# Kernel tuning notes

Hardware: AMD Instinct MI355X
Metric: run time of the kernel (lower is better)

The kernel has to match this reference:

```python
import jax, jax.numpy as jnp
import numpy as np


def _run_stacked_lstm(x, init_hc, params):
    """x: [B,T,E]; init_hc: tuple of (h,c) per layer; params: tuple of (W,U,b) per layer.
    Keras LSTMCell gate order: i, f, g(candidate), o; sigmoid recurrent act, tanh act."""
    def step(carry, xt):
        inp = xt
        new = []
        for (h, c), (W, U, b) in zip(carry, params):
            z = inp @ W + h @ U + b                      # [B, 4*units]
            i, f, g, o = jnp.split(z, 4, axis=-1)
            c2 = jax.nn.sigmoid(f) * c + jax.nn.sigmoid(i) * jnp.tanh(g)
            h2 = jax.nn.sigmoid(o) * jnp.tanh(c2)
            new.append((h2, c2))
            inp = h2                                     # feed to next layer
        return tuple(new), inp
    carry, ys = jax.lax.scan(step, init_hc, jnp.swapaxes(x, 0, 1))
    return jnp.swapaxes(ys, 0, 1), carry                 # [B,T,units], final states


def setup_inputs() -> dict:
    key = jax.random.key(0)
    ks = jax.random.split(key, 20)
    B, T, V, E, H, L = 16, 64, 32000, 512, 512, 2
    s = 0.02
    inp = {
        'ids_1': jax.random.randint(ks[0], (B, T), 0, V),
        'ids_2': jax.random.randint(ks[1], (B, T), 0, V),
        'init_state': jax.random.normal(ks[2], (L, B, H), jnp.float32),
        'emb': jax.random.normal(ks[3], (V, E), jnp.float32) * s,
        'W1_0': jax.random.normal(ks[4], (E, 4 * H), jnp.float32) * s,
        'U1_0': jax.random.normal(ks[5], (H, 4 * H), jnp.float32) * s,
        'b1_0': jnp.zeros((4 * H,), jnp.float32),
        'W1_1': jax.random.normal(ks[6], (H, 4 * H), jnp.float32) * s,
        'U1_1': jax.random.normal(ks[7], (H, 4 * H), jnp.float32) * s,
        'b1_1': jnp.zeros((4 * H,), jnp.float32),
        'W2_0': jax.random.normal(ks[8], (E, 8 * H), jnp.float32) * s,
        'U2_0': jax.random.normal(ks[9], (2 * H, 8 * H), jnp.float32) * s,
        'b2_0': jnp.zeros((8 * H,), jnp.float32),
        'W2_1': jax.random.normal(ks[10], (2 * H, 8 * H), jnp.float32) * s,
        'U2_1': jax.random.normal(ks[11], (2 * H, 8 * H), jnp.float32) * s,
        'b2_1': jnp.zeros((8 * H,), jnp.float32),
        'Wp1': jax.random.normal(ks[12], (H, V), jnp.float32) * s,
        'bp1': jnp.zeros((V,), jnp.float32),
        'Wp2': jax.random.normal(ks[13], (2 * H, V), jnp.float32) * s,
        'bp2': jnp.zeros((V,), jnp.float32),
    }
    return inp


def reference(ids_1, ids_2, init_state, emb,
              W1_0, U1_0, b1_0, W1_1, U1_1, b1_1,
              W2_0, U2_0, b2_0, W2_1, U2_1, b2_1,
              Wp1, bp1, Wp2, bp2):
    L = init_state.shape[0]
    e1 = emb[ids_1]                                       # [B,T,E]
    e2 = emb[ids_2]
    # RNN1: initial (h,c) both set to init_state per layer
    init1 = tuple((init_state[l], init_state[l]) for l in range(L))
    p1 = ((W1_0, U1_0, b1_0), (W1_1, U1_1, b1_1))
    out1, st1 = _run_stacked_lstm(e1, init1, p1)
    logits1 = out1 @ Wp1 + bp1                            # [B,T,V]
    # RNN2: initial h = concat(init, h1_final), c = concat(init, c1_final)
    init2 = tuple((jnp.concatenate([init_state[l], st1[l][0]], axis=1),
                   jnp.concatenate([init_state[l], st1[l][1]], axis=1))
                  for l in range(L))
    p2 = ((W2_0, U2_0, b2_0), (W2_1, U2_1, b2_1))
    out2, _ = _run_stacked_lstm(e2, init2, p2)
    logits2 = out2 @ Wp2 + bp2                            # [B,T,V]
    return (logits1, logits2)
```

## Files before the change

### kernel.cpp

```cpp
#include <hip/hip_runtime.h>
#include <hip/hip_bf16.h>

#define B_ 16
#define T_ 64
#define E_ 512
#define H_ 512
#define V_ 32000

typedef __attribute__((ext_vector_type(4))) float f32x4;
typedef __attribute__((ext_vector_type(8))) short s16x8;

__device__ __forceinline__ float sigm(float x){ return 1.0f/(1.0f + __expf(-x)); }

__device__ __forceinline__ unsigned short f2bf(float x){
  unsigned int u = __float_as_uint(x);
  return (unsigned short)((u + 0x7FFFu + ((u>>16)&1u)) >> 16);
}

__device__ __forceinline__ unsigned load_coh(const unsigned* p){
  unsigned v;
  asm volatile("global_load_dword %0, %1, off sc0 sc1\n\ts_waitcnt vmcnt(0)"
               : "=v"(v) : "v"(p) : "memory");
  return v;
}
__device__ __forceinline__ void store_coh16(unsigned short* p, unsigned v){
  asm volatile("global_store_short %0, %1, off sc0 sc1" :: "v"(p), "v"(v) : "memory");
}
__device__ __forceinline__ void store_cohf(float* p, float v){
  asm volatile("global_store_dword %0, %1, off sc0 sc1" :: "v"(p), "v"(v) : "memory");
}
__device__ __forceinline__ void store_cohu(unsigned* p, unsigned v){
  asm volatile("global_store_dword %0, %1, off sc0 sc1" :: "v"(p), "v"(v) : "memory");
}

__device__ __forceinline__ void gbar3(unsigned* barb, unsigned bi1, int nblk,
                                      bool det, int myblk){
  asm volatile("s_waitcnt vmcnt(0)" ::: "memory");
  __syncthreads();
  const int tid = threadIdx.x;
  if(tid == 0) store_cohu(barb + (size_t)myblk*16, bi1);
  if(det){
    if(tid < nblk){
      const unsigned* fp = barb + (size_t)tid*16;
      while(load_coh(fp) < bi1) __builtin_amdgcn_s_sleep(1);
    }
    __syncthreads();
    if(tid < 8) store_cohu(barb + 4096 + (size_t)tid*16, bi1);
  } else {
    if(tid == 0){
      const unsigned* gp = barb + 4096 + (size_t)(myblk & 7)*16;
      while(load_coh(gp) < bi1) __builtin_amdgcn_s_sleep(1);
    }
  }
  __syncthreads();
}

__global__ void k_barinit(unsigned* bar){
  int i = blockIdx.x*256 + threadIdx.x;
  if(i < 16384) bar[i] = 0u;
}

__global__ void k_gather(const int* __restrict__ ids, const float* __restrict__ emb,
                         unsigned short* __restrict__ out){
  const int row = blockIdx.x;
  const int id  = ids[row];
  float4 v = *(const float4*)(emb + (size_t)id*E_ + threadIdx.x*4);
  ushort4 o;
  o.x = f2bf(v.x); o.y = f2bf(v.y); o.z = f2bf(v.z); o.w = f2bf(v.w);
  *(ushort4*)(out + (size_t)row*E_ + threadIdx.x*4) = o;
}

__device__ __forceinline__ void tcvt_dev(const float* __restrict__ in,
    unsigned short* __restrict__ out, int N, int Hp, int Kfull, int koff, int swz,
    int bx, int by, float (*tile)[33]){
  const int n0 = bx*32, k0 = by*32;
  const int x = threadIdx.x & 31, y = threadIdx.x >> 5;
  __syncthreads();
  #pragma unroll
  for(int i=0;i<4;i++){
    int k = y + i*8;
    tile[k][x] = in[(size_t)(k0+k)*N + n0 + x];
  }
  __syncthreads();
  #pragma unroll
  for(int i=0;i<4;i++){
    int nl = y + i*8;
    int n  = n0 + nl;
    int p  = Hp ? ((n % Hp)*4 + n / Hp) : n;
    int kk = koff + k0 + x;
    size_t idx;
    if(swz){
      int k2 = kk*2;
      int slot = ((k2>>4)&7) ^ (p&7);
      idx = (size_t)p*Kfull + (((k2 & ~127) | (slot<<4) | (k2 & 15)) >> 1);
    } else {
      idx = (size_t)p*Kfull + kk;
    }
    out[idx] = f2bf(tile[x][nl]);
  }
}

__global__ __launch_bounds__(256)
void k_tcvt(const float* __restrict__ in, unsigned short* __restrict__ out,
            int N, int Hp, int Kfull, int koff, int swz){
  __shared__ float tile[32][33];
  tcvt_dev(in, out, N, Hp, Kfull, koff, swz, blockIdx.x, blockIdx.y, tile);
}

__global__ void k_bpack(const float* __restrict__ b, float* __restrict__ out, int H, int N){
  int p = blockIdx.x*256 + threadIdx.x;
  if(p < N) out[p] = b[(p&3)*H + (p>>2)];
}

__global__ void k_init1(const float* __restrict__ init_state,
                        unsigned short* h0i, float* c0i, unsigned short* h1i, float* c1i){
  int i = blockIdx.x*256 + threadIdx.x;
  if(i >= B_*H_) return;
  float v0 = init_state[i];
  float v1 = init_state[B_*H_ + i];
  h0i[i] = f2bf(v0); c0i[i] = v0;
  h1i[i] = f2bf(v1); c1i[i] = v1;
}

__global__ void k_init2(const float* __restrict__ init_state,
                        const unsigned short* __restrict__ h0seq1,
                        const unsigned short* __restrict__ h1seq1,
                        const float* __restrict__ c0f1, const float* __restrict__ c1f1,
                        unsigned short* h20i, unsigned short* h21i,
                        float* c20i, float* c21i){
  const int l = blockIdx.y;
  int i = blockIdx.x*256 + threadIdx.x;
  if(i >= B_*2*H_) return;
  const int r = i >> 10, j = i & 1023;
  unsigned short* ho = l ? h21i : h20i;
  float* co = l ? c21i : c20i;
  if(j < H_){
    float v = init_state[(size_t)l*B_*H_ + r*H_ + j];
    ho[i] = f2bf(v); co[i] = v;
  } else {
    const unsigned short* hs = l ? h1seq1 : h0seq1;
    const float* cf = l ? c1f1 : c0f1;
    ho[i] = hs[(size_t)((T_-1)*B_ + r)*H_ + (j - H_)];
    co[i] = cf[r*H_ + (j - H_)];
  }
}

__device__ __forceinline__ void mm_tile(const unsigned short* __restrict__ A,
    const unsigned short* __restrict__ Bt, const float* __restrict__ bias,
    float* __restrict__ C, int N, int K, int bm, int bn,
    unsigned short* As, unsigned short* Bs, int remap){
  const int tid = threadIdx.x;
  const int lane = tid & 63, w = tid >> 6;
  const int wm = (w>>1)*64, wn = (w&1)*64;
  const int l15 = lane & 15, kg = lane >> 4;
  f32x4 acc[4][4] = {};
  for(int k0=0; k0<K; k0+=64){
    __syncthreads();
    #pragma unroll
    for(int ch=0; ch<4; ch++){
      int off = ch*4096 + tid*16;
      int row = off >> 7;
      int s   = ((off >> 4) & 7) ^ (row & 7);
      __builtin_amdgcn_global_load_lds(
        (const __attribute__((address_space(1))) unsigned int*)(A + (size_t)(bm+row)*K + k0 + s*8),
        (__attribute__((address_space(3))) unsigned int*)((char*)As + off), 16, 0, 0);
    }
    #pragma unroll
    for(int ch=0; ch<4; ch++){
      int off = ch*4096 + tid*16;
      int row = off >> 7;
      int s   = ((off >> 4) & 7) ^ (row & 7);
      __builtin_amdgcn_global_load_lds(
        (const __attribute__((address_space(1))) unsigned int*)(Bt + (size_t)(bn+row)*K + k0 + s*8),
        (__attribute__((address_space(3))) unsigned int*)((char*)Bs + off), 16, 0, 0);
    }
    __syncthreads();
    #pragma unroll
    for(int q=0;q<2;q++){
      s16x8 af[4], bf[4];
      #pragma unroll
      for(int mt=0;mt<4;mt++){
        int row = wm + mt*16 + l15;
        int s = (q*4 + kg) ^ (row & 7);
        af[mt] = *(const s16x8*)(As + row*64 + s*8);
      }
      #pragma unroll
      for(int nt=0;nt<4;nt++){
        int row = wn + nt*16 + l15;
        int s = (q*4 + kg) ^ (row & 7);
        bf[nt] = *(const s16x8*)(Bs + row*64 + s*8);
      }
      #pragma unroll
      for(int mt=0;mt<4;mt++)
        #pragma unroll
        for(int nt=0;nt<4;nt++)
          acc[mt][nt] = __builtin_amdgcn_mfma_f32_16x16x32_bf16(af[mt], bf[nt], acc[mt][nt], 0, 0, 0);
    }
  }
  #pragma unroll
  for(int mt=0;mt<4;mt++){
    #pragma unroll
    for(int nt=0;nt<4;nt++){
      int col = bn + wn + nt*16 + l15;
      float bv = bias ? bias[col] : 0.f;
      #pragma unroll
      for(int e=0;e<4;e++){
        int row = bm + wm + mt*16 + kg*4 + e;
        int orow = remap ? ((row & 15)*T_ + (row >> 4)) : row;
        C[(size_t)orow*N + col] = acc[mt][nt][e] + bv;
      }
    }
  }
}

template<int BF32>
__global__ __launch_bounds__(256)
void k_mm(const unsigned short* __restrict__ A, const void* __restrict__ Bsrc,
          const float* __restrict__ bias, float* __restrict__ C,
          int M, int N, int K, int remap){
  __shared__ __align__(16) unsigned short As[128*64];
  __shared__ __align__(16) unsigned short Bs[128*64];
  if(!BF32){
    mm_tile(A, (const unsigned short*)Bsrc, bias, C, N, K,
            blockIdx.y*128, blockIdx.x*128, As, Bs, remap);
    return;
  }
  const int tid = threadIdx.x;
  const int lane = tid & 63, w = tid >> 6;
  const int wm = (w>>1)*64, wn = (w&1)*64;
  const int bm = blockIdx.y*128, bn = blockIdx.x*128;
  const int l15 = lane & 15, kg = lane >> 4;
  f32x4 acc[4][4] = {};
  for(int k0=0; k0<K; k0+=64){
    __syncthreads();
    #pragma unroll
    for(int ch=0; ch<4; ch++){
      int off = ch*4096 + tid*16;
      int row = off >> 7;
      int s   = ((off >> 4) & 7) ^ (row & 7);
      __builtin_amdgcn_global_load_lds(
        (const __attribute__((address_space(1))) unsigned int*)(A + (size_t)(bm+row)*K + k0 + s*8),
        (__attribute__((address_space(3))) unsigned int*)((char*)As + off), 16, 0, 0);
    }
    {
      const float* Bf = (const float*)Bsrc;
      #pragma unroll
      for(int i=0;i<8;i++){
        int kl = (tid>>5) + i*8;
        int nl = (tid&31)*4;
        float4 v = *(const float4*)(Bf + (size_t)(k0+kl)*N + bn + nl);
        int slot = kl >> 3, kb = kl & 7;
        float vv[4] = {v.x, v.y, v.z, v.w};
        #pragma unroll
        for(int jj=0;jj<4;jj++){
          int n = nl + jj;
          Bs[n*64 + ((slot ^ (n&7))*8) + kb] = f2bf(vv[jj]);
        }
      }
    }
    __syncthreads();
    #pragma unroll
    for(int q=0;q<2;q++){
      s16x8 af[4], bf[4];
      #pragma unroll
      for(int mt=0;mt<4;mt++){
        int row = wm + mt*16 + l15;
        int s = (q*4 + kg) ^ (row & 7);
        af[mt] = *(const s16x8*)(As + row*64 + s*8);
      }
      #pragma unroll
      for(int nt=0;nt<4;nt++){
        int row = wn + nt*16 + l15;
        int s = (q*4 + kg) ^ (row & 7);
        bf[nt] = *(const s16x8*)(Bs + row*64 + s*8);
      }
      #pragma unroll
      for(int mt=0;mt<4;mt++)
        #pragma unroll
        for(int nt=0;nt<4;nt++)
          acc[mt][nt] = __builtin_amdgcn_mfma_f32_16x16x32_bf16(af[mt], bf[nt], acc[mt][nt], 0, 0, 0);
    }
  }
  #pragma unroll
  for(int mt=0;mt<4;mt++){
    #pragma unroll
    for(int nt=0;nt<4;nt++){
      int col = bn + wn + nt*16 + l15;
      float bv = bias ? bias[col] : 0.f;
      #pragma unroll
      for(int e=0;e<4;e++){
        int row = bm + wm + mt*16 + kg*4 + e;
        int orow = remap ? ((row & 15)*T_ + (row >> 4)) : row;
        C[(size_t)orow*N + col] = acc[mt][nt][e] + bv;
      }
    }
  }
}

template<int C, int K, int LAYER, int HU, int TB>
__device__ __forceinline__ void rnn_body(
    unsigned short* __restrict__ Uld, float* __restrict__ zp,
    const unsigned short* __restrict__ Uslice,
    const float* __restrict__ xw0, const float* __restrict__ bpk,
    const unsigned short* __restrict__ h0init, const unsigned short* __restrict__ h1init,
    const float* __restrict__ cinit,
    unsigned short* __restrict__ h0seq, unsigned short* __restrict__ h1seq,
    float* __restrict__ cfin, unsigned* bar, int cb, int nblk, bool det, int myblk)
{
  constexpr int KW = K/4, KS = KW/32, FR = C/16, UB = C/4;
  constexpr int K2 = K*2;
  constexpr int ITEMS = 16*UB;
  const int tid = threadIdx.x;
  const int lane = tid & 63, w = tid >> 6;
  const int l15 = lane & 15, kg = lane >> 4;

  constexpr int CP = (C*K2)/4096;
  #pragma unroll
  for(int i=0;i<CP;i++){
    __builtin_amdgcn_global_load_lds(
      (const __attribute__((address_space(1))) unsigned int*)((const char*)Uslice + i*4096 + tid*16),
      (__attribute__((address_space(3))) unsigned int*)((char*)Uld + i*4096 + tid*16), 16, 0, 0);
  }
  const int base_p = cb*C;
  const int base_u = cb*UB;
  float4 bvr = make_float4(0.f,0.f,0.f,0.f);
  int er = 0, eu = 0;
  if(tid < ITEMS){ er = tid / UB; eu = tid - er*UB; bvr = *(const float4*)(bpk + base_p + eu*4); }
  float creg = 0.f;
  unsigned short* hseqW = LAYER ? h1seq : h0seq;

  int cbyte[FR], cx[FR];
  #pragma unroll
  for(int f=0;f<FR;f++){ int c = f*16 + l15; cbyte[f] = c*K2; cx[f] = (c&7)<<4; }

  __syncthreads();

  for(int it = 0; it <= T_; ++it){
    const bool active = LAYER ? (it >= 1) : (it < T_);
    const int t = LAYER ? it-1 : it;
    if(active){
      const unsigned short* asrc;
      if constexpr(LAYER == 0){
        asrc = (t == 0) ? (h0init + l15*HU)
             : (h0seq + ((size_t)(TB ? ((t-1)*B_ + l15) : (l15*T_ + (t-1))))*HU);
      } else {
        if(w < 2){
          asrc = h0seq + ((size_t)(TB ? (t*B_ + l15) : (l15*T_ + t)))*HU;
        } else {
          asrc = ((t == 0) ? (h1init + l15*HU)
               : (h1seq + ((size_t)(TB ? ((t-1)*B_ + l15) : (l15*T_ + (t-1))))*HU)) - HU;
        }
      }
      f32x4 acc[FR];
      #pragma unroll
      for(int f=0;f<FR;f++) acc[f] = (f32x4){0.f,0.f,0.f,0.f};
      #pragma unroll
      for(int s=0;s<KS;s++){
        const int kel = w*KW + s*32 + kg*8;
        s16x8 a = *(const s16x8*)(asrc + kel);
        const int kb  = kel*2;
        const int kch = kb & ~127;
        const int ksl = (kb >> 4) & 7;
        #pragma unroll
        for(int f=0;f<FR;f++){
          const int ad = cbyte[f] + kch + ((ksl<<4) ^ cx[f]);
          s16x8 b = *(const s16x8*)((const char*)Uld + ad);
          acc[f] = __builtin_amdgcn_mfma_f32_16x16x32_bf16(a, b, acc[f], 0, 0, 0);
        }
      }
      #pragma unroll
      for(int f=0;f<FR;f++)
        #pragma unroll
        for(int e=0;e<4;e++)
          zp[(w*16 + kg*4 + e)*68 + f*16 + l15] = acc[f][e];
    }
    __syncthreads();
    if(active && tid < ITEMS){
      float4 z0 = *(const float4*)(zp + (     er)*68 + eu*4);
      float4 z1 = *(const float4*)(zp + (16 + er)*68 + eu*4);
      float4 z2 = *(const float4*)(zp + (32 + er)*68 + eu*4);
      float4 z3 = *(const float4*)(zp + (48 + er)*68 + eu*4);
      float si = z0.x+z1.x+z2.x+z3.x + bvr.x;
      float sf = z0.y+z1.y+z2.y+z3.y + bvr.y;
      float sg = z0.z+z1.z+z2.z+z3.z + bvr.z;
      float so = z0.w+z1.w+z2.w+z3.w + bvr.w;
      if constexpr(LAYER == 0){
        float4 xv = *(const float4*)(xw0 + ((size_t)(er*T_ + t))*(4*HU) + base_p + eu*4);
        si += xv.x; sf += xv.y; sg += xv.z; so += xv.w;
      }
      float cin = (t == 0) ? cinit[er*HU + base_u + eu] : creg;
      float c2 = sigm(sf)*cin + sigm(si)*tanhf(sg);
      float h2 = sigm(so)*tanhf(c2);
      creg = c2;
      size_t hrow = TB ? ((size_t)(t*B_ + er)) : ((size_t)(er*T_ + t));
      store_coh16(&hseqW[hrow*HU + base_u + eu], (unsigned)f2bf(h2));
      if(t == T_-1) store_cohf(&cfin[er*HU + base_u + eu], c2);
    }
    if(it < T_) gbar3(bar, (unsigned)(it+1), nblk, det, myblk);
  }
  asm volatile("s_waitcnt vmcnt(0)" ::: "memory");
  __syncthreads();
  if(tid == 0) store_cohu(bar + (size_t)myblk*16, (unsigned)(T_+1));
}

__global__ __launch_bounds__(256, 1)
void k_rnn1m(const unsigned short* __restrict__ Ut0, const unsigned short* __restrict__ WU1,
    const float* __restrict__ xw0, const float* __restrict__ bpk0, const float* __restrict__ bpk1,
    const unsigned short* __restrict__ h0init, const unsigned short* __restrict__ h1init,
    const float* __restrict__ c0init, const float* __restrict__ c1init,
    unsigned short* __restrict__ h0seq, unsigned short* __restrict__ h1seq,
    float* __restrict__ c0fin, float* __restrict__ c1fin, unsigned* bar,
    const int* __restrict__ ids2, const float* __restrict__ emb, unsigned short* __restrict__ ebuf2,
    const float* __restrict__ b2_0, const float* __restrict__ b2_1,
    float* __restrict__ bpk20, float* __restrict__ bpk21,
    const float* __restrict__ U2_0, unsigned short* __restrict__ ut0_2,
    const float* __restrict__ W2_0, unsigned short* __restrict__ wtmp2,
    const float* __restrict__ W2_1, const float* __restrict__ U2_1, unsigned short* __restrict__ wu1_2,
    const float* __restrict__ Wp1, unsigned short* __restrict__ wpT1,
    const float* __restrict__ bp1, float* __restrict__ out1, int wide)
{
  constexpr int HU = 512, C0 = 64, C1 = 64;
  constexpr int NB0 = 4*HU/C0;
  constexpr int NRNN = NB0 + 4*HU/C1;
  constexpr int NS = 256 - NRNN;
  __shared__ __align__(16) unsigned short Uld[65536];
  __shared__ __align__(16) float zred[64*68];
  const int blk = blockIdx.x;
  const int tid = threadIdx.x;
  if(blk < NB0){
    rnn_body<C0, HU, 0, HU, 1>(Uld, zred, Ut0 + (size_t)blk*C0*HU, xw0, bpk0,
        h0init, h1init, c0init, h0seq, h1seq, c0fin, bar, blk, NRNN, blk==0, blk);
  } else if(blk < NRNN){
    rnn_body<C1, 2*HU, 1, HU, 1>(Uld, zred, WU1 + (size_t)(blk-NB0)*C1*2*HU, nullptr, bpk1,
        h0init, h1init, c1init, h0seq, h1seq, c1fin, bar, blk-NB0, NRNN, false, blk);
  } else {
    const int q = blk - NRNN;
    float (*tile)[33] = (float(*)[33])Uld;
    unsigned short* As = Uld;
    unsigned short* Bs = Uld + 8192;
    volatile int* rdy = (volatile int*)((char*)Uld + 128000);
    const int J0 = 512, J1 = J0+32, J2 = J1+4096, J3 = J2+2048, J4 = J3+4096, J5 = J4+4096;
    const int totJ = wide ? (J5 + 16000) : J5;
    for(int j = q; j < totJ; j += NS){
      if(j < J0){
        int row = j*2 + (tid>>7);
        int id = ids2[row];
        float4 v = *(const float4*)(emb + (size_t)id*E_ + (tid&127)*4);
        ushort4 o; o.x=f2bf(v.x); o.y=f2bf(v.y); o.z=f2bf(v.z); o.w=f2bf(v.w);
        *(ushort4*)(ebuf2 + (size_t)row*E_ + (tid&127)*4) = o;
      } else if(j < J1){
        int jj = j - J0;
        const float* b = (jj < 16) ? b2_0 : b2_1;
        float* o = (jj < 16) ? bpk20 : bpk21;
        int p = (jj & 15)*256 + tid;
        o[p] = b[(p&3)*1024 + (p>>2)];
      } else if(j < J2){
        int r = j - J1; tcvt_dev(U2_0, ut0_2, 4096, 1024, 1024, 0, 1, r%128, r/128, tile);
      } else if(j < J3){
        int r = j - J2; tcvt_dev(W2_0, wtmp2, 4096, 1024, 512, 0, 0, r%128, r/128, tile);
      } else if(j < J4){
        int r = j - J3; tcvt_dev(W2_1, wu1_2, 4096, 1024, 2048, 0, 1, r%128, r/128, tile);
      } else if(j < J5){
        int r = j - J4; tcvt_dev(U2_1, wu1_2, 4096, 1024, 2048, 1024, 1, r%128, r/128, tile);
      } else {
        int r = j - J5; tcvt_dev(Wp1, wpT1, 32000, 0, 512, 0, 0, r%1000, r/1000, tile);
      }
    }
    if(!wide) return;
    __syncthreads();
    __threadfence();
    if(tid == 0)
      __hip_atomic_fetch_add(bar + 5120, 1u, __ATOMIC_RELAXED, __HIP_MEMORY_SCOPE_AGENT);
    if(tid == 0){
      while(load_coh(bar + 5120) < (unsigned)NS) __builtin_amdgcn_s_sleep(8);
    }
    __syncthreads();
    for(int g = 0; g < 8; ++g){
      const unsigned req = 8u*(unsigned)g + 9u;
      for(;;){
        if(tid == 0) *rdy = 1;
        __syncthreads();
        if(tid < 32){
          if(load_coh(bar + (size_t)(NB0 + tid)*16) < req) *rdy = 0;
        }
        __syncthreads();
        if(*rdy) break;
        __builtin_amdgcn_s_sleep(16);
      }
      for(int n = q; n < 250; n += NS)
        mm_tile(h1seq, wpT1, bp1, out1, V_, 512, g*128, n*128, As, Bs, 1);
    }
  }
}

template<int HU, int C0, int C1>
__global__ __launch_bounds__(256, 1)
void k_rnn(const unsigned short* __restrict__ Ut0, const unsigned short* __restrict__ WU1,
           const float* __restrict__ xw0, const float* __restrict__ bpk0, const float* __restrict__ bpk1,
           const unsigned short* __restrict__ h0init, const unsigned short* __restrict__ h1init,
           const float* __restrict__ c0init, const float* __restrict__ c1init,
           unsigned short* __restrict__ h0seq, unsigned short* __restrict__ h1seq,
           float* __restrict__ c0fin, float* __restrict__ c1fin, unsigned* bar)
{
  constexpr int NB0 = 4*HU/C0;
  constexpr int UMAXE = (C0*HU > C1*2*HU) ? C0*HU : C1*2*HU;
  __shared__ __align__(16) unsigned short Uld[UMAXE];
  __shared__ __align__(16) float zred[64*68];
  const int nblk = gridDim.x;
  const bool det = (blockIdx.x == 0);
  const int blk = blockIdx.x;
  if(blk < NB0)
    rnn_body<C0, HU, 0, HU, 0>(Uld, zred, Ut0 + (size_t)blk*C0*HU, xw0, bpk0,
                               h0init, h1init, c0init, h0seq, h1seq, c0fin, bar, blk, nblk, det, blk);
  else
    rnn_body<C1, 2*HU, 1, HU, 0>(Uld, zred, WU1 + (size_t)(blk-NB0)*C1*2*HU, nullptr, bpk1,
                               h0init, h1init, c1init, h0seq, h1seq, c1fin, bar, blk-NB0, nblk, det, blk);
}

extern "C" void kernel_launch(void* const* d_in, const int* in_sizes, int n_in,
                              void* d_out, int out_size, void* d_ws, size_t ws_size,
                              hipStream_t stream){
  const int*   ids1 = (const int*)d_in[0];
  const int*   ids2 = (const int*)d_in[1];
  const float* init = (const float*)d_in[2];
  const float* emb  = (const float*)d_in[3];
  const float* W1_0 = (const float*)d_in[4];
  const float* U1_0 = (const float*)d_in[5];
  const float* b1_0 = (const float*)d_in[6];
  const float* W1_1 = (const float*)d_in[7];
  const float* U1_1 = (const float*)d_in[8];
  const float* b1_1 = (const float*)d_in[9];
  const float* W2_0 = (const float*)d_in[10];
  const float* U2_0 = (const float*)d_in[11];
  const float* b2_0 = (const float*)d_in[12];
  const float* W2_1 = (const float*)d_in[13];
  const float* U2_1 = (const float*)d_in[14];
  const float* b2_1 = (const float*)d_in[15];
  const float* Wp1  = (const float*)d_in[16];
  const float* bp1  = (const float*)d_in[17];
  const float* Wp2  = (const float*)d_in[18];
  const float* bp2  = (const float*)d_in[19];
  float* out1 = (float*)d_out;
  float* out2 = out1 + (size_t)B_*T_*V_;

  char* base = (char*)d_ws;
  float*          xw    = (float*)(base);
  unsigned short* ut0_1 = (unsigned short*)(base + (16u<<20));
  unsigned short* wu1_1 = (unsigned short*)(base + (18u<<20));
  unsigned short* ut0_2 = (unsigned short*)(base + (22u<<20));
  unsigned short* wu1_2 = (unsigned short*)(base + (30u<<20));
  unsigned short* wtmp  = (unsigned short*)(base + (46u<<20));
  unsigned short* ebuf  = (unsigned short*)(base + (50u<<20));
  unsigned short* h0s1  = (unsigned short*)(base + (51u<<20));
  unsigned short* h1s1  = (unsigned short*)(base + (52u<<20));
  unsigned short* h0s2  = (unsigned short*)(base + (53u<<20));
  unsigned short* h1s2  = (unsigned short*)(base + (55u<<20));
  char* M = base + (57u<<20);
  unsigned short* h0i1 = (unsigned short*)(M);
  unsigned short* h1i1 = (unsigned short*)(M + 16384);
  float* c0i1 = (float*)(M + 32768);
  float* c1i1 = (float*)(M + 65536);
  unsigned short* h2i0 = (unsigned short*)(M + 98304);
  unsigned short* h2i1 = (unsigned short*)(M + 131072);
  float* c2i0 = (float*)(M + 163840);
  float* c2i1 = (float*)(M + 229376);
  float* c0f1 = (float*)(M + 294912);
  float* c1f1 = (float*)(M + 327680);
  float* c0f2 = (float*)(M + 360448);
  float* c1f2 = (float*)(M + 425984);
  float* bpk10 = (float*)(M + 491520);
  float* bpk11 = (float*)(M + 499712);
  float* bpk20 = (float*)(M + 507904);
  float* bpk21 = (float*)(M + 524288);
  unsigned* bar1 = (unsigned*)(M + 540672);
  unsigned* bar2 = (unsigned*)(M + 540672 + 32768);
  unsigned short* wpT1 = (unsigned short*)(base + (58u<<20));
  unsigned short* wpT2 = (unsigned short*)(base + (90u<<20));
  const size_t NEED_ALL = ((size_t)90u<<20) + (size_t)V_*1024*2;
  const bool wide = ws_size >= NEED_ALL;

  k_barinit<<<dim3(64), dim3(256), 0, stream>>>(bar1);

  k_init1<<<dim3(32), dim3(256), 0, stream>>>(init, h0i1, c0i1, h1i1, c1i1);
  k_gather<<<dim3(B_*T_), dim3(128), 0, stream>>>(ids1, emb, ebuf);
  k_tcvt<<<dim3(64, 16), dim3(256), 0, stream>>>(U1_0, ut0_1, 2048, 512, 512, 0, 1);
  k_tcvt<<<dim3(64, 16), dim3(256), 0, stream>>>(W1_0, wtmp,  2048, 512, 512, 0, 0);
  k_tcvt<<<dim3(64, 16), dim3(256), 0, stream>>>(W1_1, wu1_1, 2048, 512, 1024, 0, 1);
  k_tcvt<<<dim3(64, 16), dim3(256), 0, stream>>>(U1_1, wu1_1, 2048, 512, 1024, 512, 1);
  k_bpack<<<dim3(8),  dim3(256), 0, stream>>>(b1_0, bpk10, 512, 2048);
  k_bpack<<<dim3(8),  dim3(256), 0, stream>>>(b1_1, bpk11, 512, 2048);
  k_mm<0><<<dim3(16, 8), dim3(256), 0, stream>>>(ebuf, wtmp, nullptr, xw, 1024, 2048, 512, 0);

  k_rnn1m<<<dim3(256), dim3(256), 0, stream>>>(ut0_1, wu1_1, xw, bpk10, bpk11,
      h0i1, h1i1, c0i1, c1i1, h0s1, h1s1, c0f1, c1f1, bar1,
      ids2, emb, ebuf, b2_0, b2_1, bpk20, bpk21,
      U2_0, ut0_2, W2_0, wtmp, W2_1, U2_1, wu1_2, Wp1, wpT1, bp1, out1, (int)wide);

  if(!wide){
    k_mm<1><<<dim3(250, 8), dim3(256), 0, stream>>>(h1s1, Wp1, bp1, out1, 1024, V_, 512, 1);
  }

  k_mm<0><<<dim3(32, 8), dim3(256), 0, stream>>>(ebuf, wtmp, nullptr, xw, 1024, 4096, 512, 0);
  k_init2<<<dim3(64, 2), dim3(256), 0, stream>>>(init, h0s1, h1s1, c0f1, c1f1,
                                                 h2i0, h2i1, c2i0, c2i1);
  if(wide){
    k_tcvt<<<dim3(1000, 32), dim3(256), 0, stream>>>(Wp2, wpT2, V_, 0, 1024, 0, 0);
  }

  k_rnn<1024, 64, 32><<<dim3(192), dim3(256), 0, stream>>>(ut0_2, wu1_2, xw, bpk20, bpk21,
      h2i0, h2i1, c2i0, c2i1, h0s2, h1s2, c0f2, c1f2, bar2);

  if(wide){
    k_mm<0><<<dim3(250, 8), dim3(256), 0, stream>>>(h1s2, wpT2, bp2, out2, 1024, V_, 1024, 0);
  } else {
    k_mm<1><<<dim3(250, 8), dim3(256), 0, stream>>>(h1s2, Wp2, bp2, out2, 1024, V_, 1024, 0);
  }
}
```

Before: 891.3 us.

## Overlap RNN2 with Wp2 conversion and early projection tiles in persistent kernel

Turns the second RNN kernel into a persistent kernel with 64 extra blocks, mirroring what the first RNN kernel already does. While the recurrence runs, those blocks transpose-convert Wp2 to bf16 and then compute the first two 128-row groups of the output projection as soon as enough timesteps are ready. The later projection GEMM only covers the remaining rows. The change removes the separate conversion launch and hides part of the projection behind the latency-bound recurrence, at the cost of extra spin-wait synchronisation and of competing with the RNN blocks for memory bandwidth.

```diff
diff --git a/kernel.cpp b/kernel.cpp
--- a/kernel.cpp
+++ b/kernel.cpp
@@ -217,18 +217,18 @@
 __global__ __launch_bounds__(256)
 void k_mm(const unsigned short* __restrict__ A, const void* __restrict__ Bsrc,
           const float* __restrict__ bias, float* __restrict__ C,
-          int M, int N, int K, int remap){
+          int M, int N, int K, int remap, int bm0){
   __shared__ __align__(16) unsigned short As[128*64];
   __shared__ __align__(16) unsigned short Bs[128*64];
   if(!BF32){
     mm_tile(A, (const unsigned short*)Bsrc, bias, C, N, K,
-            blockIdx.y*128, blockIdx.x*128, As, Bs, remap);
+            bm0 + blockIdx.y*128, blockIdx.x*128, As, Bs, remap);
     return;
   }
   const int tid = threadIdx.x;
   const int lane = tid & 63, w = tid >> 6;
   const int wm = (w>>1)*64, wn = (w&1)*64;
-  const int bm = blockIdx.y*128, bn = blockIdx.x*128;
+  const int bm = bm0 + blockIdx.y*128, bn = blockIdx.x*128;
   const int l15 = lane & 15, kg = lane >> 4;
   f32x4 acc[4][4] = {};
   for(int k0=0; k0<K; k0+=64){
@@ -493,28 +493,62 @@
   }
 }
 
-template<int HU, int C0, int C1>
 __global__ __launch_bounds__(256, 1)
-void k_rnn(const unsigned short* __restrict__ Ut0, const unsigned short* __restrict__ WU1,
-           const float* __restrict__ xw0, const float* __restrict__ bpk0, const float* __restrict__ bpk1,
-           const unsigned short* __restrict__ h0init, const unsigned short* __restrict__ h1init,
-           const float* __restrict__ c0init, const float* __restrict__ c1init,
-           unsigned short* __restrict__ h0seq, unsigned short* __restrict__ h1seq,
-           float* __restrict__ c0fin, float* __restrict__ c1fin, unsigned* bar)
+void k_rnn2m(const unsigned short* __restrict__ Ut0, const unsigned short* __restrict__ WU1,
+    const float* __restrict__ xw0, const float* __restrict__ bpk0, const float* __restrict__ bpk1,
+    const unsigned short* __restrict__ h0init, const unsigned short* __restrict__ h1init,
+    const float* __restrict__ c0init, const float* __restrict__ c1init,
+    unsigned short* __restrict__ h0seq, unsigned short* __restrict__ h1seq,
+    float* __restrict__ c0fin, float* __restrict__ c1fin, unsigned* bar,
+    const float* __restrict__ Wp2, unsigned short* __restrict__ wpT2,
+    const float* __restrict__ bp2, float* __restrict__ out2, int wide)
 {
+  constexpr int HU = 1024, C0 = 64, C1 = 32;
   constexpr int NB0 = 4*HU/C0;
-  constexpr int UMAXE = (C0*HU > C1*2*HU) ? C0*HU : C1*2*HU;
-  __shared__ __align__(16) unsigned short Uld[UMAXE];
+  constexpr int NRNN = NB0 + 4*HU/C1;
+  constexpr int NS = 64;
+  __shared__ __align__(16) unsigned short Uld[65536];
   __shared__ __align__(16) float zred[64*68];
-  const int nblk = gridDim.x;
-  const bool det = (blockIdx.x == 0);
   const int blk = blockIdx.x;
-  if(blk < NB0)
-    rnn_body<C0, HU, 0, HU, 0>(Uld, zred, Ut0 + (size_t)blk*C0*HU, xw0, bpk0,
-                               h0init, h1init, c0init, h0seq, h1seq, c0fin, bar, blk, nblk, det, blk);
-  else
-    rnn_body<C1, 2*HU, 1, HU, 0>(Uld, zred, WU1 + (size_t)(blk-NB0)*C1*2*HU, nullptr, bpk1,
-                               h0init, h1init, c1init, h0seq, h1seq, c1fin, bar, blk-NB0, nblk, det, blk);
+  const int tid = threadIdx.x;
+  if(blk < NB0){
+    rnn_body<C0, HU, 0, HU, 1>(Uld, zred, Ut0 + (size_t)blk*C0*HU, xw0, bpk0,
+        h0init, h1init, c0init, h0seq, h1seq, c0fin, bar, blk, NRNN, blk==0, blk);
+  } else if(blk < NRNN){
+    rnn_body<C1, 2*HU, 1, HU, 1>(Uld, zred, WU1 + (size_t)(blk-NB0)*C1*2*HU, nullptr, bpk1,
+        h0init, h1init, c1init, h0seq, h1seq, c1fin, bar, blk-NB0, NRNN, false, blk);
+  } else if(wide){
+    const int q = blk - NRNN;
+    float (*tile)[33] = (float(*)[33])Uld;
+    unsigned short* As = Uld;
+    unsigned short* Bs = Uld + 8192;
+    volatile int* rdy = (volatile int*)((char*)Uld + 128000);
+    for(int j = q; j < 32000; j += NS)
+      tcvt_dev(Wp2, wpT2, 32000, 0, 1024, 0, 0, j%1000, j/1000, tile);
+    __syncthreads();
+    __threadfence();
+    if(tid == 0)
+      __hip_atomic_fetch_add(bar + 5120, 1u, __ATOMIC_RELAXED, __HIP_MEMORY_SCOPE_AGENT);
+    if(tid == 0){
+      while(load_coh(bar + 5120) < (unsigned)NS) __builtin_amdgcn_s_sleep(8);
+    }
+    __syncthreads();
+    for(int g = 0; g < 2; ++g){
+      const unsigned req = 8u*(unsigned)g + 9u;
+      for(;;){
+        if(tid == 0) *rdy = 1;
+        __syncthreads();
+        if(tid < 128){
+          if(load_coh(bar + (size_t)(NB0 + tid)*16) < req) *rdy = 0;
+        }
+        __syncthreads();
+        if(*rdy) break;
+        __builtin_amdgcn_s_sleep(16);
+      }
+      for(int n = q; n < 250; n += NS)
+        mm_tile(h1seq, wpT2, bp2, out2, V_, 1024, g*128, n*128, As, Bs, 1);
+    }
+  }
 }
 
 extern "C" void kernel_launch(void* const* d_in, const int* in_sizes, int n_in,
@@ -589,7 +623,7 @@
   k_tcvt<<<dim3(64, 16), dim3(256), 0, stream>>>(U1_1, wu1_1, 2048, 512, 1024, 512, 1);
   k_bpack<<<dim3(8),  dim3(256), 0, stream>>>(b1_0, bpk10, 512, 2048);
   k_bpack<<<dim3(8),  dim3(256), 0, stream>>>(b1_1, bpk11, 512, 2048);
-  k_mm<0><<<dim3(16, 8), dim3(256), 0, stream>>>(ebuf, wtmp, nullptr, xw, 1024, 2048, 512, 0);
+  k_mm<0><<<dim3(16, 8), dim3(256), 0, stream>>>(ebuf, wtmp, nullptr, xw, 1024, 2048, 512, 0, 0);
 
   k_rnn1m<<<dim3(256), dim3(256), 0, stream>>>(ut0_1, wu1_1, xw, bpk10, bpk11,
       h0i1, h1i1, c0i1, c1i1, h0s1, h1s1, c0f1, c1f1, bar1,
@@ -597,22 +631,20 @@
       U2_0, ut0_2, W2_0, wtmp, W2_1, U2_1, wu1_2, Wp1, wpT1, bp1, out1, (int)wide);
 
   if(!wide){
-    k_mm<1><<<dim3(250, 8), dim3(256), 0, stream>>>(h1s1, Wp1, bp1, out1, 1024, V_, 512, 1);
-  }
-
-  k_mm<0><<<dim3(32, 8), dim3(256), 0, stream>>>(ebuf, wtmp, nullptr, xw, 1024, 4096, 512, 0);
+    k_mm<1><<<dim3(250, 8), dim3(256), 0, stream>>>(h1s1, Wp1, bp1, out1, 1024, V_, 512, 1, 0);
+  }
+
+  k_mm<0><<<dim3(32, 8), dim3(256), 0, stream>>>(ebuf, wtmp, nullptr, xw, 1024, 4096, 512, 0, 0);
   k_init2<<<dim3(64, 2), dim3(256), 0, stream>>>(init, h0s1, h1s1, c0f1, c1f1,
                                                  h2i0, h2i1, c2i0, c2i1);
+
+  k_rnn2m<<<dim3(256), dim3(256), 0, stream>>>(ut0_2, wu1_2, xw, bpk20, bpk21,
+      h2i0, h2i1, c2i0, c2i1, h0s2, h1s2, c0f2, c1f2, bar2,
+      Wp2, wpT2, bp2, out2, (int)wide);
+
   if(wide){
-    k_tcvt<<<dim3(1000, 32), dim3(256), 0, stream>>>(Wp2, wpT2, V_, 0, 1024, 0, 0);
-  }
-
-  k_rnn<1024, 64, 32><<<dim3(192), dim3(256), 0, stream>>>(ut0_2, wu1_2, xw, bpk20, bpk21,
-      h2i0, h2i1, c2i0, c2i1, h0s2, h1s2, c0f2, c1f2, bar2);
-
-  if(wide){
-    k_mm<0><<<dim3(250, 8), dim3(256), 0, stream>>>(h1s2, wpT2, bp2, out2, 1024, V_, 1024, 0);
+    k_mm<0><<<dim3(250, 6), dim3(256), 0, stream>>>(h1s2, wpT2, bp2, out2, 1024, V_, 1024, 1, 256);
   } else {
-    k_mm<1><<<dim3(250, 8), dim3(256), 0, stream>>>(h1s2, Wp2, bp2, out2, 1024, V_, 1024, 0);
-  }
-}
+    k_mm<1><<<dim3(250, 8), dim3(256), 0, stream>>>(h1s2, Wp2, bp2, out2, 1024, V_, 1024, 1, 0);
+  }
+}
```

Measured after the change: 1.034 ms. 1.16x slower.
